# Performance work log

Hardware: AMD Instinct MI355X
Metric: run time of the kernel (lower is better)

Reference implementation:

```python
import jax, jax.numpy as jnp
import numpy as np
import math

N = 4096
E = 131072
IN_DIM, HID, OUT = 512, 256, 64
DEPTH = 3
RATIO = 0.5


def setup_inputs() -> dict:
    key = jax.random.key(0)
    ks = jax.random.split(key, 12)

    def w(k, fi, fo):
        return jax.random.normal(k, (fi, fo), jnp.float32) * (1.0 / np.sqrt(fi).astype(np.float32))

    return {
        "x": jax.random.normal(ks[0], (N, IN_DIM), jnp.float32),
        "edge_index": jax.random.randint(ks[1], (2, E), 0, N, jnp.int32),
        "dW0": w(ks[2], IN_DIM, HID), "dW1": w(ks[3], HID, HID),
        "dW2": w(ks[4], HID, HID), "dW3": w(ks[5], HID, HID),
        "db0": jnp.zeros((HID,), jnp.float32), "db1": jnp.zeros((HID,), jnp.float32),
        "db2": jnp.zeros((HID,), jnp.float32), "db3": jnp.zeros((HID,), jnp.float32),
        "pw0": jax.random.normal(ks[6], (HID,), jnp.float32),
        "pw1": jax.random.normal(ks[7], (HID,), jnp.float32),
        "pw2": jax.random.normal(ks[8], (HID,), jnp.float32),
        "uW0": w(ks[9], HID, HID), "uW1": w(ks[10], HID, HID), "uW2": w(ks[11], HID, OUT),
        "ub0": jnp.zeros((HID,), jnp.float32), "ub1": jnp.zeros((HID,), jnp.float32),
        "ub2": jnp.zeros((OUT,), jnp.float32),
    }


def gcn_conv(x, A, W, b):
    # GCNConv(improved=True): A_hat = A + 2I, sym-normalized.
    n = A.shape[0]
    eye = jnp.eye(n, dtype=A.dtype)
    Ah = A + 2.0 * eye
    d = Ah.sum(axis=1)
    dinv = jnp.where(d > 0, jax.lax.rsqrt(d), 0.0)
    An = dinv[:, None] * Ah * dinv[None, :]
    return An @ (x @ W) + b


def augment_adj(A):
    # add self loops, square the (weighted) adjacency, remove self loops
    n = A.shape[0]
    eye = jnp.eye(n, dtype=A.dtype)
    Al = A + eye
    A2 = Al @ Al
    return A2 * (1.0 - eye)


def topk_pool(x, A, w, k):
    # TopKPooling: score = tanh(x.w/||w||); keep top-k; gate kept features by score.
    score = jnp.tanh((x @ w) / jnp.linalg.norm(w))
    _, perm = jax.lax.top_k(score, k)
    xp = x[perm] * score[perm][:, None]
    return xp, A[perm][:, perm], perm


def _forward(x, edge_index, down_Ws, down_bs, pool_ws, up_Ws, up_bs):
    A = jnp.zeros((N, N), jnp.float32).at[edge_index[0], edge_index[1]].set(1.0)
    x = jax.nn.relu(gcn_conv(x, A, down_Ws[0], down_bs[0]))
    xs, As, perms = [x], [A], []
    n = N
    for i in range(1, DEPTH + 1):
        A = augment_adj(A)
        k = int(math.ceil(RATIO * n)); n = k
        x, A, perm = topk_pool(x, A, pool_ws[i - 1], k)
        x = jax.nn.relu(gcn_conv(x, A, down_Ws[i], down_bs[i]))
        if i < DEPTH:
            xs.append(x); As.append(A)
        perms.append(perm)
    for i in range(DEPTH):
        j = DEPTH - 1 - i
        res, A, perm = xs[j], As[j], perms[j]
        up = jnp.zeros_like(res).at[perm].set(x)   # unpool (sum_res=True)
        x = res + up
        x = gcn_conv(x, A, up_Ws[i], up_bs[i])
        if i < DEPTH - 1:
            x = jax.nn.relu(x)
    return x


def reference(x, edge_index, dW0, dW1, dW2, dW3, db0, db1, db2, db3,
              pw0, pw1, pw2, uW0, uW1, uW2, ub0, ub1, ub2):
    return _forward(x, edge_index,
                    [dW0, dW1, dW2, dW3], [db0, db1, db2, db3],
                    [pw0, pw1, pw2],
                    [uW0, uW1, uW2], [ub0, ub1, ub2])
```

## Files before the change

kernel.cpp:

```cpp
#include <hip/hip_runtime.h>
#include <math.h>

#define NN 4096
#define EE 131072
#define IN_DIM 512
#define HID 256
#define OUT_DIM 64
#define ECAP 128

typedef __attribute__((ext_vector_type(8))) short bf8_t;
typedef __attribute__((ext_vector_type(4))) float f4_t;
typedef __attribute__((ext_vector_type(8))) unsigned short us8_t;

#define GAS __attribute__((address_space(1)))
#define LAS __attribute__((address_space(3)))

__device__ __forceinline__ unsigned short f2bf(float v){
  union { float f; unsigned u; } x; x.f = v;
  unsigned r = x.u + 0x7fffu + ((x.u >> 16) & 1u);
  return (unsigned short)(r >> 16);
}
__device__ __forceinline__ float bf2f(unsigned short h){
  union { float f; unsigned u; } x; x.u = ((unsigned)h) << 16;
  return x.f;
}

__device__ __forceinline__ float waveReduceSum(float v){
#pragma unroll
  for (int off = 32; off > 0; off >>= 1) v += __shfl_down(v, off);
  return v;
}

__global__ __launch_bounds__(256) void k_prep(
    const float* __restrict__ x_in, const float* __restrict__ dW0,
    const float* __restrict__ dW1, const float* __restrict__ dW2,
    const float* __restrict__ dW3, const float* __restrict__ uW0,
    const float* __restrict__ uW1, const float* __restrict__ uW2,
    unsigned* __restrict__ bits,
    unsigned short* __restrict__ xinh, unsigned short* __restrict__ xinl,
    unsigned short* __restrict__ W0th, unsigned short* __restrict__ W0tl,
    unsigned short* __restrict__ W5th, unsigned short* __restrict__ W5tl,
    unsigned short* __restrict__ W2th, unsigned short* __restrict__ W2tl)
{
  int b = blockIdx.x;
  if (b < 128){
    int base = b * 4096 + threadIdx.x;
#pragma unroll
    for (int i = 0; i < 16; ++i) bits[base + i * 256] = 0;
    return;
  }
  b -= 128;
  if (b < 2048){
    int i0 = b * 1024 + threadIdx.x;
#pragma unroll
    for (int i = 0; i < 4; ++i){
      int idx = i0 + i * 256;
      float v = x_in[idx];
      unsigned short h = f2bf(v);
      xinh[idx] = h; xinl[idx] = f2bf(v - bf2f(h));
    }
    return;
  }
  b -= 2048;
  const float* X; unsigned short *Th, *Tl; int R, C, tile;
  if (b < 128){ X = dW0; Th = W0th; Tl = W0tl; R = 512; C = 256; tile = b; }
  else if (b < 448){
    int t2 = b - 128; int z = t2 >> 6; int rem = t2 & 63;
    const float* ws[5] = {dW1, dW2, dW3, uW0, uW1};
    X = ws[z]; Th = W5th + (size_t)z * 65536; Tl = W5tl + (size_t)z * 65536;
    R = 256; C = 256; tile = rem;
  } else { X = uW2; Th = W2th; Tl = W2tl; R = 256; C = 64; tile = b - 448; }
  int tpr = C >> 5;
  int bx = (tile % tpr) * 32, by = (tile / tpr) * 32;
  __shared__ float t[32][33];
  int tx = threadIdx.x & 31, ty = threadIdx.x >> 5;
#pragma unroll
  for (int i = 0; i < 4; ++i)
    t[ty + i * 8][tx] = X[(size_t)(by + ty + i * 8) * C + bx + tx];
  __syncthreads();
#pragma unroll
  for (int i = 0; i < 4; ++i){
    float v = t[tx][ty + i * 8];
    unsigned short h = f2bf(v);
    size_t o = (size_t)(bx + ty + i * 8) * R + by + tx;
    Th[o] = h; Tl[o] = f2bf(v - bf2f(h));
  }
}

__global__ void k_build_bits(const int* __restrict__ ei, unsigned* __restrict__ bits){
  int e = blockIdx.x * blockDim.x + threadIdx.x;
  if (e < EE){
    int r = ei[e], c = ei[EE + e];
    atomicOr(&bits[r * 128 + (c >> 5)], 1u << (c & 31));
  }
}

__global__ __launch_bounds__(128) void k_ell(const unsigned* __restrict__ bits,
                                             int* __restrict__ ell, int* __restrict__ cnt,
                                             float* __restrict__ dinv){
  int r = blockIdx.x, t = threadIdx.x;
  unsigned w = bits[r * 128 + t];
  int c = __popc(w);
  __shared__ int sc[128];
  sc[t] = c; __syncthreads();
  for (int off = 1; off < 128; off <<= 1){
    int a = sc[t], b = (t >= off) ? sc[t - off] : 0;
    __syncthreads(); sc[t] = a + b; __syncthreads();
  }
  int total = sc[127];
  int pos = sc[t] - c;
  int base = r * ECAP;
  while (w){
    int b = __ffs(w) - 1; w &= w - 1;
    if (pos < ECAP) ell[base + pos] = t * 32 + b;
    pos++;
  }
  if (t == 0){
    cnt[r] = (total < ECAP) ? total : ECAP;
    dinv[r] = 1.0f / sqrtf((float)total + 2.0f);
  }
}

template<int NCOLS, int RELU, int SC>
__global__ __launch_bounds__(256) void k_spmm_ell(
    const int* __restrict__ ell, const int* __restrict__ cnt,
    const float* __restrict__ Zs, const float* __restrict__ dinv,
    const float* __restrict__ bias, float* __restrict__ out,
    const float* __restrict__ scw, float* __restrict__ score)
{
  int r = blockIdx.x;
  __shared__ int s_idx[ECAP];
  __shared__ int s_n;
  __shared__ float sh[4 * NCOLS];
  __shared__ float sd[4], sq[4];
  if (threadIdx.x == 0) s_n = cnt[r];
  for (int i = threadIdx.x; i < ECAP; i += 256) s_idx[i] = ell[r * ECAP + i];
  __syncthreads();
  int n = s_n; if (n > ECAP) n = ECAP;
  int wv = threadIdx.x >> 6, lane = threadIdx.x & 63;
  if (NCOLS == 256){
    f4_t acc = (f4_t){0.f, 0.f, 0.f, 0.f};
    for (int e = wv; e < n; e += 4){
      const f4_t* row = (const f4_t*)(Zs + (size_t)s_idx[e] * 256);
      acc += row[lane];
    }
    ((f4_t*)(sh + wv * 256))[lane] = acc;
  } else {
    float acc = 0.f;
    for (int e = wv; e < n; e += 4)
      acc += Zs[(size_t)s_idx[e] * 64 + lane];
    sh[wv * 64 + lane] = acc;
  }
  __syncthreads();
  int t = threadIdx.x;
  float o = 0.f;
  if (t < NCOLS){
    float y = sh[t] + sh[NCOLS + t] + sh[2 * NCOLS + t] + sh[3 * NCOLS + t];
    float z = Zs[(size_t)r * NCOLS + t];
    o = dinv[r] * (y + 2.0f * z) + bias[t];
    if (RELU) o = fmaxf(o, 0.f);
    out[(size_t)r * NCOLS + t] = o;
  }
  if (SC){
    float w = scw[t];
    float d = waveReduceSum(o * w);
    float q = waveReduceSum(w * w);
    if (!lane){ sd[wv] = d; sq[wv] = q; }
    __syncthreads();
    if (!t) score[r] = tanhf((sd[0] + sd[1] + sd[2] + sd[3]) / sqrtf(sq[0] + sq[1] + sq[2] + sq[3]));
  }
}

__global__ __launch_bounds__(256) void k_pool_build(
    const float* __restrict__ x0, const float* __restrict__ score,
    const int* __restrict__ perm1, const int* __restrict__ inv1,
    const int* __restrict__ ell, const int* __restrict__ cnt,
    unsigned short* __restrict__ xph, unsigned short* __restrict__ xpl,
    unsigned char* __restrict__ Rb,
    unsigned short* __restrict__ xu1h, unsigned short* __restrict__ xu1l)
{
  int b = blockIdx.x;
  if (b < 2048){
    int pr = perm1[b]; float s = score[pr];
    int c = threadIdx.x;
    float v = x0[(size_t)pr * 256 + c] * s;
    unsigned short h = f2bf(v);
    xph[(size_t)b * 256 + c] = h;
    xpl[(size_t)b * 256 + c] = f2bf(v - bf2f(h));
    return;
  }
  if (b < 6144){
    int k = b - 2048;
    __shared__ unsigned char row[2048];
    for (int i = threadIdx.x; i < 512; i += 256) ((int*)row)[i] = 0;
    __syncthreads();
    int n = cnt[k];
    for (int e = threadIdx.x; e < n; e += 256){
      int s = inv1[ell[k * ECAP + e]];
      if (s >= 0) row[s] = 1;
    }
    __syncthreads();
    if (threadIdx.x == 0){
      int sk = inv1[k];
      if (sk >= 0) row[sk] += 1;
    }
    __syncthreads();
    *(uint2*)(Rb + (size_t)k * 2048 + threadIdx.x * 8) = *(uint2*)(row + threadIdx.x * 8);
    return;
  }
  int r = b - 6144;
  if (inv1[r] < 0){
    int c = threadIdx.x;
    float v = x0[(size_t)r * 256 + c];
    unsigned short h = f2bf(v);
    xu1h[(size_t)r * 256 + c] = h;
    xu1l[(size_t)r * 256 + c] = f2bf(v - bf2f(h));
  }
}

__global__ __launch_bounds__(256) void k_pool_fill(
    const float* __restrict__ x, const float* __restrict__ score,
    const int* __restrict__ perm, const int* __restrict__ inv, int k,
    unsigned short* __restrict__ xph, unsigned short* __restrict__ xpl,
    unsigned short* __restrict__ xuh, unsigned short* __restrict__ xul)
{
  int b = blockIdx.x, c = threadIdx.x;
  if (b < k){
    int pr = perm[b]; float s = score[pr];
    float v = x[(size_t)pr * 256 + c] * s;
    unsigned short h = f2bf(v);
    xph[(size_t)b * 256 + c] = h;
    xpl[(size_t)b * 256 + c] = f2bf(v - bf2f(h));
  } else {
    int r = b - k;
    if (inv[r] < 0){
      float v = x[(size_t)r * 256 + c];
      unsigned short h = f2bf(v);
      xuh[(size_t)r * 256 + c] = h;
      xul[(size_t)r * 256 + c] = f2bf(v - bf2f(h));
    }
  }
}

__global__ __launch_bounds__(256) void k_sq1(const int* __restrict__ ell, const int* __restrict__ cnt,
                                             const int* __restrict__ perm,
                                             const unsigned char* __restrict__ Rb,
                                             unsigned short* __restrict__ A1h,
                                             float* __restrict__ dinv1){
  int r = blockIdx.x;
  int pr = perm[r];
  __shared__ int s_idx[ECAP];
  __shared__ int s_n;
  __shared__ float sred[4];
  if (threadIdx.x == 0) s_n = cnt[pr];
  for (int i = threadIdx.x; i < ECAP; i += 256) s_idx[i] = ell[pr * ECAP + i];
  __syncthreads();
  int n = s_n; if (n > ECAP) n = ECAP;
  int colb = threadIdx.x * 8;
  uint2 acc = *(const uint2*)(Rb + (size_t)pr * 2048 + colb);
  for (int e = 0; e < n; ++e){
    uint2 v = *(const uint2*)(Rb + (size_t)s_idx[e] * 2048 + colb);
    acc.x += v.x; acc.y += v.y;
  }
  float fs = 0.f;
  us8_t o;
#pragma unroll
  for (int j = 0; j < 8; ++j){
    unsigned byte = ((j < 4 ? acc.x : acc.y) >> (8 * (j & 3))) & 0xFFu;
    if (colb + j == r) byte = 0;
    float f = (float)byte;
    fs += f;
    o[j] = f2bf(f);
  }
  *(us8_t*)(A1h + (size_t)r * 2048 + colb) = o;
  fs = waveReduceSum(fs);
  int lane = threadIdx.x & 63, wd = threadIdx.x >> 6;
  if (!lane) sred[wd] = fs;
  __syncthreads();
  if (!threadIdx.x)
    dinv1[r] = 1.0f / sqrtf(sred[0] + sred[1] + sred[2] + sred[3] + 2.0f);
}

template<int TWO>
__global__ __launch_bounds__(256) void k_tr_b(const unsigned short* __restrict__ Sh,
                                              const unsigned short* __restrict__ Sl,
                                              unsigned short* __restrict__ Dh,
                                              unsigned short* __restrict__ Dl, int R, int C){
  __shared__ unsigned short th[32][33];
  __shared__ unsigned short tl[TWO ? 32 : 1][TWO ? 33 : 1];
  int bx = blockIdx.x * 32, by = blockIdx.y * 32;
  int tx = threadIdx.x & 31, ty = threadIdx.x >> 5;
#pragma unroll
  for (int i = 0; i < 4; ++i){
    th[ty + i * 8][tx] = Sh[(size_t)(by + ty + i * 8) * C + bx + tx];
    if (TWO) tl[ty + i * 8][tx] = Sl[(size_t)(by + ty + i * 8) * C + bx + tx];
  }
  __syncthreads();
#pragma unroll
  for (int i = 0; i < 4; ++i){
    size_t o = (size_t)(bx + ty + i * 8) * R + by + tx;
    Dh[o] = th[tx][ty + i * 8];
    if (TWO) Dl[o] = tl[tx][ty + i * 8];
  }
}

template<int SRCL, int OUTL>
__global__ void k_grow2(const unsigned short* __restrict__ Sh, const unsigned short* __restrict__ Sl,
                        const unsigned short* __restrict__ Th, const unsigned short* __restrict__ Tl,
                        const int* __restrict__ perm,
                        unsigned short* __restrict__ Lh, unsigned short* __restrict__ Ll,
                        unsigned short* __restrict__ Rh, unsigned short* __restrict__ Rl,
                        int n, int half)
{
  int b = blockIdx.x;
  const unsigned short *sh, *sl; unsigned short *dh, *dl; int r;
  if (b < half){ r = b; sh = Sh; sl = Sl; dh = Lh; dl = Ll; }
  else { r = b - half; sh = Th; sl = Tl; dh = Rh; dl = Rl; }
  int pr = perm[r];
  for (int c = threadIdx.x; c < n; c += 256){
    float v = bf2f(sh[(size_t)pr * n + c]);
    if (SRCL) v += bf2f(sl[(size_t)pr * n + c]);
    if (pr == c) v += 1.f;
    unsigned short h = f2bf(v);
    dh[(size_t)r * n + c] = h;
    if (OUTL) dl[(size_t)r * n + c] = f2bf(v - bf2f(h));
  }
}

template<int HAS_AL, int HAS_BL, int HAS_LL, int EPI>
__global__ __launch_bounds__(256) void k_mm(
    const unsigned short* __restrict__ Ah, const unsigned short* __restrict__ Al,
    const unsigned short* __restrict__ Bh, const unsigned short* __restrict__ Bl,
    int M, int N, int K, int KS, float* __restrict__ P,
    float* __restrict__ Cf, unsigned short* __restrict__ Ch, unsigned short* __restrict__ Cl,
    const float* __restrict__ dinv)
{
  constexpr int NARR = 2 + HAS_AL + HAS_BL;
  constexpr int BUF = NARR * 8192;
  __shared__ int4 ldsq[NARR * 512 * 2];
  char* ldsc = (char*)ldsq;

  const int tid = threadIdx.x, lane = tid & 63, wid = tid >> 6;
  const int wm = wid >> 1, wn = wid & 1;
  const int bm = blockIdx.y << 6, bn = blockIdx.x << 6;
  const int z = blockIdx.z;
  const int l15 = lane & 15, l4 = lane >> 4;

  f4_t acc[2][2];
#pragma unroll
  for (int i = 0; i < 2; ++i)
#pragma unroll
    for (int j = 0; j < 2; ++j) acc[i][j] = (f4_t){0.f, 0.f, 0.f, 0.f};

  const size_t rb = (size_t)K * 2;
  const size_t kz = (size_t)z * KS * 2;
  const char* pAh = (const char*)Ah + (size_t)bm * rb;
  const char* pAl = HAS_AL ? (const char*)Al + (size_t)bm * rb : nullptr;
  const char* pBh = (const char*)Bh + (size_t)bn * rb;
  const char* pBl = HAS_BL ? (const char*)Bl + (size_t)bn * rb : nullptr;

  auto stage = [&](int t, int b2){
    char* ldsb = ldsc + b2 * BUF;
    const size_t kb = kz + (size_t)t * 128;
#pragma unroll
    for (int it = 0; it < 2; ++it){
      const int idx = tid + (it << 8);
      const int row = idx >> 3;
      const int kc = ((idx & 7) << 4) ^ ((row & 7) << 4);
      const size_t go = (size_t)row * rb + kb + kc;
      const int lo = idx * 16;
      __builtin_amdgcn_global_load_lds((const GAS void*)(pAh + go), (LAS void*)(ldsb + lo), 16, 0, 0);
      __builtin_amdgcn_global_load_lds((const GAS void*)(pBh + go), (LAS void*)(ldsb + 8192 + lo), 16, 0, 0);
      if (HAS_AL)
        __builtin_amdgcn_global_load_lds((const GAS void*)(pAl + go), (LAS void*)(ldsb + 16384 + lo), 16, 0, 0);
      if (HAS_BL)
        __builtin_amdgcn_global_load_lds((const GAS void*)(pBl + go), (LAS void*)(ldsb + (2 + HAS_AL) * 8192 + lo), 16, 0, 0);
    }
  };

  const int T = KS >> 6;
  stage(0, 0);
  int b = 0;
  for (int t = 0; t < T; ++t){
    if (t + 1 < T){
      stage(t + 1, b ^ 1);
      if constexpr (NARR == 2) asm volatile("s_waitcnt vmcnt(4)" ::: "memory");
      else if constexpr (NARR == 3) asm volatile("s_waitcnt vmcnt(6)" ::: "memory");
      else asm volatile("s_waitcnt vmcnt(8)" ::: "memory");
    } else {
      asm volatile("s_waitcnt vmcnt(0)" ::: "memory");
    }
    __syncthreads();
    const char* ldsb = ldsc + b * BUF;
#pragma unroll
    for (int ks = 0; ks < 2; ++ks){
      bf8_t aH[2], aL[2], bH[2], bL[2];
#pragma unroll
      for (int f = 0; f < 2; ++f){
        int ar = wm * 32 + f * 16 + l15;
        int aoff = ar * 128 + (((ks * 64) + (l4 << 4)) ^ ((ar & 7) << 4));
        aH[f] = *(const bf8_t*)(ldsb + aoff);
        if (HAS_AL) aL[f] = *(const bf8_t*)(ldsb + 16384 + aoff);
        int br = wn * 32 + f * 16 + l15;
        int boff = br * 128 + (((ks * 64) + (l4 << 4)) ^ ((br & 7) << 4));
        bH[f] = *(const bf8_t*)(ldsb + 8192 + boff);
        if (HAS_BL) bL[f] = *(const bf8_t*)(ldsb + (2 + HAS_AL) * 8192 + boff);
      }
#pragma unroll
      for (int i = 0; i < 2; ++i)
#pragma unroll
        for (int j = 0; j < 2; ++j){
          acc[i][j] = __builtin_amdgcn_mfma_f32_16x16x32_bf16(aH[i], bH[j], acc[i][j], 0, 0, 0);
          if (HAS_BL) acc[i][j] = __builtin_amdgcn_mfma_f32_16x16x32_bf16(aH[i], bL[j], acc[i][j], 0, 0, 0);
          if (HAS_AL) acc[i][j] = __builtin_amdgcn_mfma_f32_16x16x32_bf16(aL[i], bH[j], acc[i][j], 0, 0, 0);
          if (HAS_LL) acc[i][j] = __builtin_amdgcn_mfma_f32_16x16x32_bf16(aL[i], bL[j], acc[i][j], 0, 0, 0);
        }
    }
    __syncthreads();
    b ^= 1;
  }

  float* Pz = (EPI == 0) ? P + (size_t)z * M * N : nullptr;
#pragma unroll
  for (int i = 0; i < 2; ++i)
#pragma unroll
    for (int j = 0; j < 2; ++j)
#pragma unroll
      for (int r = 0; r < 4; ++r){
        int grow = bm + wm * 32 + i * 16 + l4 * 4 + r;
        int gcol = bn + wn * 32 + j * 16 + l15;
        float v = acc[i][j][r];
        size_t o = (size_t)grow * N + gcol;
        if (EPI == 0){
          Pz[o] = v;
        } else if (EPI == 2){
          Cf[o] = dinv[grow] * v;
        } else {
          float sv = dinv[grow] * v;
          Cf[o] = sv;
          unsigned short h = f2bf(sv);
          size_t ot = (size_t)gcol * M + grow;
          Ch[ot] = h; Cl[ot] = f2bf(sv - bf2f(h));
        }
      }
}

template<int EPI, int SC>
__global__ __launch_bounds__(256) void k_red(
    const float* __restrict__ P, int Z, int M, int NC,
    const float* __restrict__ dinv, const float* __restrict__ Zs,
    const float* __restrict__ bias,
    float* __restrict__ Of, unsigned short* __restrict__ Oh, unsigned short* __restrict__ Ol,
    float* __restrict__ dout, int relu,
    const float* __restrict__ scw, float* __restrict__ score,
    const float* __restrict__ res, const int* __restrict__ permsel)
{
  int row = blockIdx.x;
  int prow = (EPI == 4) ? permsel[row] : 0;
  float rsum = 0.f;
  float o_sc = 0.f;
  for (int c = threadIdx.x; c < NC; c += 256){
    size_t o = (size_t)row * NC + c;
    float s = P[o];
    for (int zz = 1; zz < Z; ++zz) s += P[(size_t)zz * M * NC + o];
    if (EPI == 2){
      float out = dinv[row] * (s + 2.0f * Zs[o]) + bias[c];
      if (relu) out = fmaxf(out, 0.f);
      Of[o] = out;
      o_sc = out;
    } else if (EPI == 3){
      float v = (c == row) ? 0.f : s;
      unsigned short h = f2bf(v);
      Oh[o] = h; Ol[o] = f2bf(v - bf2f(h));
      rsum += v;
    } else {
      float out = dinv[row] * (s + 2.0f * Zs[o]) + bias[c];
      if (relu) out = fmaxf(out, 0.f);
      float comb = res[(size_t)prow * NC + c] + out;
      unsigned short h = f2bf(comb);
      size_t od = (size_t)prow * NC + c;
      Oh[od] = h; Ol[od] = f2bf(comb - bf2f(h));
    }
  }
  int lane = threadIdx.x & 63, wd = threadIdx.x >> 6;
  if (EPI == 3){
    rsum = waveReduceSum(rsum);
    __shared__ float sr[4];
    if (!lane) sr[wd] = rsum;
    __syncthreads();
    if (!threadIdx.x) dout[row] = 1.0f / sqrtf(sr[0] + sr[1] + sr[2] + sr[3] + 2.0f);
  }
  if (SC){
    float w = scw[threadIdx.x];
    float d = waveReduceSum(o_sc * w);
    float q = waveReduceSum(w * w);
    __shared__ float sd[4], sq[4];
    if (!lane){ sd[wd] = d; sq[wd] = q; }
    __syncthreads();
    if (!threadIdx.x)
      score[row] = tanhf((sd[0] + sd[1] + sd[2] + sd[3]) / sqrtf(sq[0] + sq[1] + sq[2] + sq[3]));
  }
}

__global__ void k_topk(const float* __restrict__ score, int n, int k,
                       int* __restrict__ perm, int* __restrict__ inv){
  int i = blockIdx.x; float si = score[i];
  int cnt = 0;
  for (int j = threadIdx.x; j < n; j += 256){
    float sj = score[j];
    if (sj > si || (sj == si && j < i)) cnt++;
  }
#pragma unroll
  for (int off = 32; off > 0; off >>= 1) cnt += __shfl_down(cnt, off);
  __shared__ int sh[4];
  int lane = threadIdx.x & 63, wid = threadIdx.x >> 6;
  if (lane == 0) sh[wid] = cnt;
  __syncthreads();
  if (threadIdx.x == 0){
    int rank = sh[0] + sh[1] + sh[2] + sh[3];
    if (rank < k){ perm[rank] = i; inv[i] = rank; }
    else inv[i] = -1;
  }
}

extern "C" void kernel_launch(void* const* d_in, const int* in_sizes, int n_in,
                              void* d_out, int out_size, void* d_ws, size_t ws_size,
                              hipStream_t stream){
  (void)in_sizes; (void)n_in; (void)out_size;
  const float* x_in = (const float*)d_in[0];
  const int*   ei   = (const int*)d_in[1];
  const float* dW0 = (const float*)d_in[2];
  const float* dW1 = (const float*)d_in[3];
  const float* dW2 = (const float*)d_in[4];
  const float* dW3 = (const float*)d_in[5];
  const float* db0 = (const float*)d_in[6];
  const float* db1 = (const float*)d_in[7];
  const float* db2 = (const float*)d_in[8];
  const float* db3 = (const float*)d_in[9];
  const float* pw0 = (const float*)d_in[10];
  const float* pw1 = (const float*)d_in[11];
  const float* pw2 = (const float*)d_in[12];
  const float* uW0 = (const float*)d_in[13];
  const float* uW1 = (const float*)d_in[14];
  const float* uW2 = (const float*)d_in[15];
  const float* ub0 = (const float*)d_in[16];
  const float* ub1 = (const float*)d_in[17];
  const float* ub2 = (const float*)d_in[18];

  char* p = (char*)d_ws;
  auto alloc = [&](size_t nbytes) -> void* {
    void* q = (void*)p; p += (nbytes + 255) & ~(size_t)255; return q;
  };
  unsigned* bits = (unsigned*)alloc((size_t)4096 * 128 * 4);
  int* ell = (int*)alloc((size_t)4096 * ECAP * 4);
  int* cnt = (int*)alloc(4096 * 4);
  int* inv1 = (int*)alloc(4096 * 4);
  int* inv2 = (int*)alloc(2048 * 4);
  int* inv3 = (int*)alloc(1024 * 4);
  unsigned char* Rb = (unsigned char*)alloc((size_t)4096 * 2048);
  float* Pp = (float*)alloc((size_t)8 * 1024 * 1024);
  unsigned short* A1h = (unsigned short*)alloc((size_t)2048 * 2048 * 2);
  unsigned short* A1T = (unsigned short*)alloc((size_t)2048 * 2048 * 2);
  unsigned short* A2h = (unsigned short*)alloc((size_t)1024 * 1024 * 2);
  unsigned short* A2l = (unsigned short*)alloc((size_t)1024 * 1024 * 2);
  unsigned short* A2Th = (unsigned short*)alloc((size_t)1024 * 1024 * 2);
  unsigned short* A2Tl = (unsigned short*)alloc((size_t)1024 * 1024 * 2);
  unsigned short* A3h = (unsigned short*)alloc((size_t)512 * 512 * 2);
  unsigned short* A3l = (unsigned short*)alloc((size_t)512 * 512 * 2);
  unsigned short* Lb2h = (unsigned short*)alloc((size_t)1024 * 2048 * 2);
  unsigned short* Rt2h = (unsigned short*)alloc((size_t)1024 * 2048 * 2);
  unsigned short* Lb3h = (unsigned short*)alloc((size_t)512 * 1024 * 2);
  unsigned short* Lb3l = (unsigned short*)alloc((size_t)512 * 1024 * 2);
  unsigned short* Rt3h = (unsigned short*)alloc((size_t)512 * 1024 * 2);
  unsigned short* Rt3l = (unsigned short*)alloc((size_t)512 * 1024 * 2);
  unsigned short* xinh = (unsigned short*)alloc((size_t)4096 * 512 * 2);
  unsigned short* xinl = (unsigned short*)alloc((size_t)4096 * 512 * 2);
  float* x0 = (float*)alloc((size_t)4096 * HID * 4);
  float* x1 = (float*)alloc((size_t)2048 * HID * 4);
  float* x2 = (float*)alloc((size_t)1024 * HID * 4);
  unsigned short* xu1h = (unsigned short*)alloc((size_t)4096 * HID * 2);
  unsigned short* xu1l = (unsigned short*)alloc((size_t)4096 * HID * 2);
  unsigned short* xu2h = (unsigned short*)alloc((size_t)2048 * HID * 2);
  unsigned short* xu2l = (unsigned short*)alloc((size_t)2048 * HID * 2);
  unsigned short* xu3h = (unsigned short*)alloc((size_t)1024 * HID * 2);
  unsigned short* xu3l = (unsigned short*)alloc((size_t)1024 * HID * 2);
  unsigned short* xph = (unsigned short*)alloc((size_t)2048 * HID * 2);
  unsigned short* xpl = (unsigned short*)alloc((size_t)2048 * HID * 2);
  unsigned short* W0th = (unsigned short*)alloc((size_t)256 * 512 * 2);
  unsigned short* W0tl = (unsigned short*)alloc((size_t)256 * 512 * 2);
  unsigned short* W5th = (unsigned short*)alloc((size_t)5 * 256 * 256 * 2);
  unsigned short* W5tl = (unsigned short*)alloc((size_t)5 * 256 * 256 * 2);
  unsigned short* W2th = (unsigned short*)alloc((size_t)64 * 256 * 2);
  unsigned short* W2tl = (unsigned short*)alloc((size_t)64 * 256 * 2);
  float* Zs  = (float*)alloc((size_t)4096 * HID * 4);
  unsigned short* ZsTh = (unsigned short*)alloc((size_t)256 * 2048 * 2);
  unsigned short* ZsTl = (unsigned short*)alloc((size_t)256 * 2048 * 2);
  float* dinv0 = (float*)alloc(4096 * 4);
  float* dinv1 = (float*)alloc(2048 * 4);
  float* dinv2 = (float*)alloc(1024 * 4);
  float* dinv3 = (float*)alloc(512 * 4);
  float* score = (float*)alloc(4096 * 4);
  int* perm1 = (int*)alloc(2048 * 4);
  int* perm2 = (int*)alloc(1024 * 4);
  int* perm3 = (int*)alloc(512 * 4);
  if ((size_t)(p - (char*)d_ws) > ws_size) return;

  k_prep<<<2640, 256, 0, stream>>>(x_in, dW0, dW1, dW2, dW3, uW0, uW1, uW2, bits,
                                   xinh, xinl, W0th, W0tl, W5th, W5tl, W2th, W2tl);
  k_build_bits<<<EE / 256, 256, 0, stream>>>(ei, bits);
  k_ell<<<4096, 128, 0, stream>>>(bits, ell, cnt, dinv0);

  { dim3 g(4, 64);
    k_mm<1,1,0,2><<<g, 256, 0, stream>>>(xinh, xinl, W0th, W0tl, 4096, HID, IN_DIM, IN_DIM,
                                         nullptr, Zs, nullptr, nullptr, dinv0); }
  k_spmm_ell<256,1,1><<<4096, 256, 0, stream>>>(ell, cnt, Zs, dinv0, db0, x0, pw0, score);

  k_topk<<<4096, 256, 0, stream>>>(score, 4096, 2048, perm1, inv1);
  k_pool_build<<<10240, 256, 0, stream>>>(x0, score, perm1, inv1, ell, cnt,
                                          xph, xpl, Rb, xu1h, xu1l);
  k_sq1<<<2048, 256, 0, stream>>>(ell, cnt, perm1, Rb, A1h, dinv1);
  { dim3 g(4, 32);
    k_mm<1,1,0,4><<<g, 256, 0, stream>>>(xph, xpl, W5th, W5tl, 2048, HID, HID, HID,
                                         nullptr, Zs, ZsTh, ZsTl, dinv1); }
  { dim3 g(4, 32, 4);
    k_mm<0,1,0,0><<<g, 256, 0, stream>>>(A1h, nullptr, ZsTh, ZsTl, 2048, HID, 2048, 512,
                                         Pp, nullptr, nullptr, nullptr, nullptr); }
  k_red<2,1><<<2048, 256, 0, stream>>>(Pp, 4, 2048, 256, dinv1, Zs, db1,
                                       x1, nullptr, nullptr, nullptr, 1, pw1, score, nullptr, nullptr);

  k_topk<<<2048, 256, 0, stream>>>(score, 2048, 1024, perm2, inv2);
  { dim3 g(64, 64); k_tr_b<0><<<g, 256, 0, stream>>>(A1h, nullptr, A1T, nullptr, 2048, 2048); }
  k_grow2<0,0><<<2048, 256, 0, stream>>>(A1h, nullptr, A1T, nullptr, perm2,
                                         Lb2h, nullptr, Rt2h, nullptr, 2048, 1024);
  { dim3 g(16, 16, 2);
    k_mm<0,0,0,0><<<g, 256, 0, stream>>>(Lb2h, nullptr, Rt2h, nullptr, 1024, 1024, 2048, 1024,
                                         Pp, nullptr, nullptr, nullptr, nullptr); }
  k_red<3,0><<<1024, 256, 0, stream>>>(Pp, 2, 1024, 1024, nullptr, nullptr, nullptr,
                                       nullptr, A2h, A2l, dinv2, 0, nullptr, nullptr, nullptr, nullptr);
  k_pool_fill<<<3072, 256, 0, stream>>>(x1, score, perm2, inv2, 1024, xph, xpl, xu2h, xu2l);
  { dim3 g(4, 16);
    k_mm<1,1,0,4><<<g, 256, 0, stream>>>(xph, xpl, W5th + 65536, W5tl + 65536, 1024, HID, HID, HID,
                                         nullptr, Zs, ZsTh, ZsTl, dinv2); }
  { dim3 g(4, 16, 4);
    k_mm<1,1,0,0><<<g, 256, 0, stream>>>(A2h, A2l, ZsTh, ZsTl, 1024, HID, 1024, 256,
                                         Pp, nullptr, nullptr, nullptr, nullptr); }
  k_red<2,1><<<1024, 256, 0, stream>>>(Pp, 4, 1024, 256, dinv2, Zs, db2,
                                       x2, nullptr, nullptr, nullptr, 1, pw2, score, nullptr, nullptr);

  k_topk<<<1024, 256, 0, stream>>>(score, 1024, 512, perm3, inv3);
  { dim3 g(32, 32); k_tr_b<1><<<g, 256, 0, stream>>>(A2h, A2l, A2Th, A2Tl, 1024, 1024); }
  k_grow2<1,1><<<1024, 256, 0, stream>>>(A2h, A2l, A2Th, A2Tl, perm3,
                                         Lb3h, Lb3l, Rt3h, Rt3l, 1024, 512);
  { dim3 g(8, 8, 4);
    k_mm<1,1,1,0><<<g, 256, 0, stream>>>(Lb3h, Lb3l, Rt3h, Rt3l, 512, 512, 1024, 256,
                                         Pp, nullptr, nullptr, nullptr, nullptr); }
  k_red<3,0><<<512, 256, 0, stream>>>(Pp, 4, 512, 512, nullptr, nullptr, nullptr,
                                      nullptr, A3h, A3l, dinv3, 0, nullptr, nullptr, nullptr, nullptr);
  k_pool_fill<<<1536, 256, 0, stream>>>(x2, score, perm3, inv3, 512, xph, xpl, xu3h, xu3l);
  { dim3 g(4, 8);
    k_mm<1,1,0,4><<<g, 256, 0, stream>>>(xph, xpl, W5th + 2 * 65536, W5tl + 2 * 65536, 512, HID, HID, HID,
                                         nullptr, Zs, ZsTh, ZsTl, dinv3); }
  { dim3 g(4, 8, 4);
    k_mm<1,1,0,0><<<g, 256, 0, stream>>>(A3h, A3l, ZsTh, ZsTl, 512, HID, 512, 128,
                                         Pp, nullptr, nullptr, nullptr, nullptr); }
  k_red<4,0><<<512, 256, 0, stream>>>(Pp, 4, 512, 256, dinv3, Zs, db3,
                                      nullptr, xu3h, xu3l, nullptr, 1, nullptr, nullptr, x2, perm3);

  { dim3 g(4, 16);
    k_mm<1,1,0,4><<<g, 256, 0, stream>>>(xu3h, xu3l, W5th + 3 * 65536, W5tl + 3 * 65536, 1024, HID, HID, HID,
                                         nullptr, Zs, ZsTh, ZsTl, dinv2); }
  { dim3 g(4, 16, 4);
    k_mm<1,1,0,0><<<g, 256, 0, stream>>>(A2h, A2l, ZsTh, ZsTl, 1024, HID, 1024, 256,
                                         Pp, nullptr, nullptr, nullptr, nullptr); }
  k_red<4,0><<<1024, 256, 0, stream>>>(Pp, 4, 1024, 256, dinv2, Zs, ub0,
                                       nullptr, xu2h, xu2l, nullptr, 1, nullptr, nullptr, x1, perm2);

  { dim3 g(4, 32);
    k_mm<1,1,0,4><<<g, 256, 0, stream>>>(xu2h, xu2l, W5th + 4 * 65536, W5tl + 4 * 65536, 2048, HID, HID, HID,
                                         nullptr, Zs, ZsTh, ZsTl, dinv1); }
  { dim3 g(4, 32, 4);
    k_mm<0,1,0,0><<<g, 256, 0, stream>>>(A1h, nullptr, ZsTh, ZsTl, 2048, HID, 2048, 512,
                                         Pp, nullptr, nullptr, nullptr, nullptr); }
  k_red<4,0><<<2048, 256, 0, stream>>>(Pp, 4, 2048, 256, dinv1, Zs, ub1,
                                       nullptr, xu1h, xu1l, nullptr, 1, nullptr, nullptr, x0, perm1);

  { dim3 g(1, 64);
    k_mm<1,1,0,2><<<g, 256, 0, stream>>>(xu1h, xu1l, W2th, W2tl, 4096, OUT_DIM, HID, HID,
                                         nullptr, Zs, nullptr, nullptr, dinv0); }
  k_spmm_ell<64,0,0><<<4096, 256, 0, stream>>>(ell, cnt, Zs, dinv0, ub2, (float*)d_out, nullptr, nullptr);
}
```

Before: 243.8 us.

## Fuse pool fill, transpose and row/col gather into one kernel; vectorize reductions

Replaces the separate full-matrix transpose, the row/column gather kernel and the pool-fill kernel with a single k_pp kernel. It gathers rows directly and writes the permuted transposed columns from tiled reads, so the full transposed adjacency copy is never materialized. It also rewrites k_red to handle one row per wavefront with float4 loads, removing shared-memory block reductions and cutting the grid size by four. The fused kernel has heterogeneous block roles and scattered column writes, and it moves the pool fill earlier, before the squaring matmul.

```diff
diff --git a/kernel.cpp b/kernel.cpp
--- a/kernel.cpp
+++ b/kernel.cpp
@@ -11,6 +11,7 @@
 typedef __attribute__((ext_vector_type(8))) short bf8_t;
 typedef __attribute__((ext_vector_type(4))) float f4_t;
 typedef __attribute__((ext_vector_type(8))) unsigned short us8_t;
+typedef __attribute__((ext_vector_type(4))) unsigned short us4_t;
 
 #define GAS __attribute__((address_space(1)))
 #define LAS __attribute__((address_space(3)))
@@ -218,12 +219,18 @@
   }
 }
 
-__global__ __launch_bounds__(256) void k_pool_fill(
+template<int SRCL, int OUTL>
+__global__ __launch_bounds__(256) void k_pp(
     const float* __restrict__ x, const float* __restrict__ score,
-    const int* __restrict__ perm, const int* __restrict__ inv, int k,
+    const int* __restrict__ perm, const int* __restrict__ inv, int n, int k,
     unsigned short* __restrict__ xph, unsigned short* __restrict__ xpl,
-    unsigned short* __restrict__ xuh, unsigned short* __restrict__ xul)
+    unsigned short* __restrict__ xuh, unsigned short* __restrict__ xul,
+    const unsigned short* __restrict__ Ah, const unsigned short* __restrict__ Al,
+    unsigned short* __restrict__ Lh, unsigned short* __restrict__ Ll,
+    unsigned short* __restrict__ Rh, unsigned short* __restrict__ Rl)
 {
+  __shared__ float t[32][33];
+  __shared__ int sinv[32];
   int b = blockIdx.x, c = threadIdx.x;
   if (b < k){
     int pr = perm[b]; float s = score[pr];
@@ -231,13 +238,56 @@
     unsigned short h = f2bf(v);
     xph[(size_t)b * 256 + c] = h;
     xpl[(size_t)b * 256 + c] = f2bf(v - bf2f(h));
-  } else {
-    int r = b - k;
-    if (inv[r] < 0){
-      float v = x[(size_t)r * 256 + c];
+    return;
+  }
+  b -= k;
+  if (b < n){
+    if (inv[b] < 0){
+      float v = x[(size_t)b * 256 + c];
       unsigned short h = f2bf(v);
-      xuh[(size_t)r * 256 + c] = h;
-      xul[(size_t)r * 256 + c] = f2bf(v - bf2f(h));
+      xuh[(size_t)b * 256 + c] = h;
+      xul[(size_t)b * 256 + c] = f2bf(v - bf2f(h));
+    }
+    return;
+  }
+  b -= n;
+  if (b < k){
+    int r = b, pr = perm[r];
+    for (int cc = threadIdx.x; cc < n; cc += 256){
+      float v = bf2f(Ah[(size_t)pr * n + cc]);
+      if (SRCL) v += bf2f(Al[(size_t)pr * n + cc]);
+      if (pr == cc) v += 1.f;
+      unsigned short h = f2bf(v);
+      Lh[(size_t)r * n + cc] = h;
+      if (OUTL) Ll[(size_t)r * n + cc] = f2bf(v - bf2f(h));
+    }
+    return;
+  }
+  b -= k;
+  int tpr = n >> 5;
+  int kt = b / tpr, ct = b - kt * tpr;
+  int tx = threadIdx.x & 31, ty = threadIdx.x >> 5;
+  if (threadIdx.x < 32) sinv[threadIdx.x] = inv[ct * 32 + threadIdx.x];
+#pragma unroll
+  for (int i = 0; i < 4; ++i){
+    int kl = ty + i * 8;
+    size_t src = (size_t)(kt * 32 + kl) * n + ct * 32 + tx;
+    float v = bf2f(Ah[src]);
+    if (SRCL) v += bf2f(Al[src]);
+    t[kl][tx] = v;
+  }
+  __syncthreads();
+#pragma unroll
+  for (int i = 0; i < 4; ++i){
+    int cl = ty + i * 8;
+    int s = sinv[cl];
+    if (s >= 0){
+      float v = t[tx][cl];
+      if (kt * 32 + tx == ct * 32 + cl) v += 1.f;
+      unsigned short h = f2bf(v);
+      size_t o = (size_t)s * n + kt * 32 + tx;
+      Rh[o] = h;
+      if (OUTL) Rl[o] = f2bf(v - bf2f(h));
     }
   }
 }
@@ -281,52 +331,6 @@
     dinv1[r] = 1.0f / sqrtf(sred[0] + sred[1] + sred[2] + sred[3] + 2.0f);
 }
 
-template<int TWO>
-__global__ __launch_bounds__(256) void k_tr_b(const unsigned short* __restrict__ Sh,
-                                              const unsigned short* __restrict__ Sl,
-                                              unsigned short* __restrict__ Dh,
-                                              unsigned short* __restrict__ Dl, int R, int C){
-  __shared__ unsigned short th[32][33];
-  __shared__ unsigned short tl[TWO ? 32 : 1][TWO ? 33 : 1];
-  int bx = blockIdx.x * 32, by = blockIdx.y * 32;
-  int tx = threadIdx.x & 31, ty = threadIdx.x >> 5;
-#pragma unroll
-  for (int i = 0; i < 4; ++i){
-    th[ty + i * 8][tx] = Sh[(size_t)(by + ty + i * 8) * C + bx + tx];
-    if (TWO) tl[ty + i * 8][tx] = Sl[(size_t)(by + ty + i * 8) * C + bx + tx];
-  }
-  __syncthreads();
-#pragma unroll
-  for (int i = 0; i < 4; ++i){
-    size_t o = (size_t)(bx + ty + i * 8) * R + by + tx;
-    Dh[o] = th[tx][ty + i * 8];
-    if (TWO) Dl[o] = tl[tx][ty + i * 8];
-  }
-}
-
-template<int SRCL, int OUTL>
-__global__ void k_grow2(const unsigned short* __restrict__ Sh, const unsigned short* __restrict__ Sl,
-                        const unsigned short* __restrict__ Th, const unsigned short* __restrict__ Tl,
-                        const int* __restrict__ perm,
-                        unsigned short* __restrict__ Lh, unsigned short* __restrict__ Ll,
-                        unsigned short* __restrict__ Rh, unsigned short* __restrict__ Rl,
-                        int n, int half)
-{
-  int b = blockIdx.x;
-  const unsigned short *sh, *sl; unsigned short *dh, *dl; int r;
-  if (b < half){ r = b; sh = Sh; sl = Sl; dh = Lh; dl = Ll; }
-  else { r = b - half; sh = Th; sl = Tl; dh = Rh; dl = Rl; }
-  int pr = perm[r];
-  for (int c = threadIdx.x; c < n; c += 256){
-    float v = bf2f(sh[(size_t)pr * n + c]);
-    if (SRCL) v += bf2f(sl[(size_t)pr * n + c]);
-    if (pr == c) v += 1.f;
-    unsigned short h = f2bf(v);
-    dh[(size_t)r * n + c] = h;
-    if (OUTL) dl[(size_t)r * n + c] = f2bf(v - bf2f(h));
-  }
-}
-
 template<int HAS_AL, int HAS_BL, int HAS_LL, int EPI>
 __global__ __launch_bounds__(256) void k_mm(
     const unsigned short* __restrict__ Ah, const unsigned short* __restrict__ Al,
@@ -455,50 +459,68 @@
     const float* __restrict__ scw, float* __restrict__ score,
     const float* __restrict__ res, const int* __restrict__ permsel)
 {
-  int row = blockIdx.x;
+  int w = threadIdx.x >> 6, lane = threadIdx.x & 63;
+  int row = blockIdx.x * 4 + w;
   int prow = (EPI == 4) ? permsel[row] : 0;
-  float rsum = 0.f;
-  float o_sc = 0.f;
-  for (int c = threadIdx.x; c < NC; c += 256){
-    size_t o = (size_t)row * NC + c;
-    float s = P[o];
-    for (int zz = 1; zz < Z; ++zz) s += P[(size_t)zz * M * NC + o];
+  float di = (EPI != 3) ? dinv[row] : 0.f;
+  float rsum = 0.f, o_d = 0.f, o_q = 0.f;
+  for (int c0 = lane * 4; c0 < NC; c0 += 256){
+    size_t o = (size_t)row * NC + c0;
+    f4_t s = *(const f4_t*)(P + o);
+    for (int zz = 1; zz < Z; ++zz) s += *(const f4_t*)(P + (size_t)zz * M * NC + o);
     if (EPI == 2){
-      float out = dinv[row] * (s + 2.0f * Zs[o]) + bias[c];
-      if (relu) out = fmaxf(out, 0.f);
-      Of[o] = out;
-      o_sc = out;
+      f4_t z4 = *(const f4_t*)(Zs + o);
+      f4_t b4 = *(const f4_t*)(bias + c0);
+      f4_t out;
+#pragma unroll
+      for (int j = 0; j < 4; ++j){
+        float v = di * (s[j] + 2.0f * z4[j]) + b4[j];
+        if (relu) v = fmaxf(v, 0.f);
+        out[j] = v;
+      }
+      *(f4_t*)(Of + o) = out;
+      if (SC){
+        f4_t w4 = *(const f4_t*)(scw + c0);
+#pragma unroll
+        for (int j = 0; j < 4; ++j){ o_d += out[j] * w4[j]; o_q += w4[j] * w4[j]; }
+      }
     } else if (EPI == 3){
-      float v = (c == row) ? 0.f : s;
-      unsigned short h = f2bf(v);
-      Oh[o] = h; Ol[o] = f2bf(v - bf2f(h));
-      rsum += v;
+      us4_t h4, l4v;
+#pragma unroll
+      for (int j = 0; j < 4; ++j){
+        float v = (c0 + j == row) ? 0.f : s[j];
+        unsigned short h = f2bf(v);
+        h4[j] = h; l4v[j] = f2bf(v - bf2f(h));
+        rsum += v;
+      }
+      *(us4_t*)(Oh + o) = h4;
+      *(us4_t*)(Ol + o) = l4v;
     } else {
-      float out = dinv[row] * (s + 2.0f * Zs[o]) + bias[c];
-      if (relu) out = fmaxf(out, 0.f);
-      float comb = res[(size_t)prow * NC + c] + out;
-      unsigned short h = f2bf(comb);
-      size_t od = (size_t)prow * NC + c;
-      Oh[od] = h; Ol[od] = f2bf(comb - bf2f(h));
-    }
-  }
-  int lane = threadIdx.x & 63, wd = threadIdx.x >> 6;
+      f4_t z4 = *(const f4_t*)(Zs + o);
+      f4_t b4 = *(const f4_t*)(bias + c0);
+      f4_t r4 = *(const f4_t*)(res + (size_t)prow * NC + c0);
+      us4_t h4, l4v;
+#pragma unroll
+      for (int j = 0; j < 4; ++j){
+        float v = di * (s[j] + 2.0f * z4[j]) + b4[j];
+        if (relu) v = fmaxf(v, 0.f);
+        float comb = r4[j] + v;
+        unsigned short h = f2bf(comb);
+        h4[j] = h; l4v[j] = f2bf(comb - bf2f(h));
+      }
+      size_t od = (size_t)prow * NC + c0;
+      *(us4_t*)(Oh + od) = h4;
+      *(us4_t*)(Ol + od) = l4v;
+    }
+  }
   if (EPI == 3){
     rsum = waveReduceSum(rsum);
-    __shared__ float sr[4];
-    if (!lane) sr[wd] = rsum;
-    __syncthreads();
-    if (!threadIdx.x) dout[row] = 1.0f / sqrtf(sr[0] + sr[1] + sr[2] + sr[3] + 2.0f);
+    if (!lane) dout[row] = 1.0f / sqrtf(rsum + 2.0f);
   }
   if (SC){
-    float w = scw[threadIdx.x];
-    float d = waveReduceSum(o_sc * w);
-    float q = waveReduceSum(w * w);
-    __shared__ float sd[4], sq[4];
-    if (!lane){ sd[wd] = d; sq[wd] = q; }
-    __syncthreads();
-    if (!threadIdx.x)
-      score[row] = tanhf((sd[0] + sd[1] + sd[2] + sd[3]) / sqrtf(sq[0] + sq[1] + sq[2] + sq[3]));
+    o_d = waveReduceSum(o_d);
+    o_q = waveReduceSum(o_q);
+    if (!lane) score[row] = tanhf(o_d / sqrtf(o_q));
   }
 }
 
@@ -560,11 +582,8 @@
   unsigned char* Rb = (unsigned char*)alloc((size_t)4096 * 2048);
   float* Pp = (float*)alloc((size_t)8 * 1024 * 1024);
   unsigned short* A1h = (unsigned short*)alloc((size_t)2048 * 2048 * 2);
-  unsigned short* A1T = (unsigned short*)alloc((size_t)2048 * 2048 * 2);
   unsigned short* A2h = (unsigned short*)alloc((size_t)1024 * 1024 * 2);
   unsigned short* A2l = (unsigned short*)alloc((size_t)1024 * 1024 * 2);
-  unsigned short* A2Th = (unsigned short*)alloc((size_t)1024 * 1024 * 2);
-  unsigned short* A2Tl = (unsigned short*)alloc((size_t)1024 * 1024 * 2);
   unsigned short* A3h = (unsigned short*)alloc((size_t)512 * 512 * 2);
   unsigned short* A3l = (unsigned short*)alloc((size_t)512 * 512 * 2);
   unsigned short* Lb2h = (unsigned short*)alloc((size_t)1024 * 2048 * 2);
@@ -625,45 +644,43 @@
   { dim3 g(4, 32, 4);
     k_mm<0,1,0,0><<<g, 256, 0, stream>>>(A1h, nullptr, ZsTh, ZsTl, 2048, HID, 2048, 512,
                                          Pp, nullptr, nullptr, nullptr, nullptr); }
-  k_red<2,1><<<2048, 256, 0, stream>>>(Pp, 4, 2048, 256, dinv1, Zs, db1,
-                                       x1, nullptr, nullptr, nullptr, 1, pw1, score, nullptr, nullptr);
+  k_red<2,1><<<512, 256, 0, stream>>>(Pp, 4, 2048, 256, dinv1, Zs, db1,
+                                      x1, nullptr, nullptr, nullptr, 1, pw1, score, nullptr, nullptr);
 
   k_topk<<<2048, 256, 0, stream>>>(score, 2048, 1024, perm2, inv2);
-  { dim3 g(64, 64); k_tr_b<0><<<g, 256, 0, stream>>>(A1h, nullptr, A1T, nullptr, 2048, 2048); }
-  k_grow2<0,0><<<2048, 256, 0, stream>>>(A1h, nullptr, A1T, nullptr, perm2,
-                                         Lb2h, nullptr, Rt2h, nullptr, 2048, 1024);
+  k_pp<0,0><<<8192, 256, 0, stream>>>(x1, score, perm2, inv2, 2048, 1024,
+                                      xph, xpl, xu2h, xu2l, A1h, nullptr,
+                                      Lb2h, nullptr, Rt2h, nullptr);
   { dim3 g(16, 16, 2);
     k_mm<0,0,0,0><<<g, 256, 0, stream>>>(Lb2h, nullptr, Rt2h, nullptr, 1024, 1024, 2048, 1024,
                                          Pp, nullptr, nullptr, nullptr, nullptr); }
-  k_red<3,0><<<1024, 256, 0, stream>>>(Pp, 2, 1024, 1024, nullptr, nullptr, nullptr,
-                                       nullptr, A2h, A2l, dinv2, 0, nullptr, nullptr, nullptr, nullptr);
-  k_pool_fill<<<3072, 256, 0, stream>>>(x1, score, perm2, inv2, 1024, xph, xpl, xu2h, xu2l);
+  k_red<3,0><<<256, 256, 0, stream>>>(Pp, 2, 1024, 1024, nullptr, nullptr, nullptr,
+                                      nullptr, A2h, A2l, dinv2, 0, nullptr, nullptr, nullptr, nullptr);
   { dim3 g(4, 16);
     k_mm<1,1,0,4><<<g, 256, 0, stream>>>(xph, xpl, W5th + 65536, W5tl + 65536, 1024, HID, HID, HID,
                                          nullptr, Zs, ZsTh, ZsTl, dinv2); }
   { dim3 g(4, 16, 4);
     k_mm<1,1,0,0><<<g, 256, 0, stream>>>(A2h, A2l, ZsTh, ZsTl, 1024, HID, 1024, 256,
                                          Pp, nullptr, nullptr, nullptr, nullptr); }
-  k_red<2,1><<<1024, 256, 0, stream>>>(Pp, 4, 1024, 256, dinv2, Zs, db2,
-                                       x2, nullptr, nullptr, nullptr, 1, pw2, score, nullptr, nullptr);
+  k_red<2,1><<<256, 256, 0, stream>>>(Pp, 4, 1024, 256, dinv2, Zs, db2,
+                                      x2, nullptr, nullptr, nullptr, 1, pw2, score, nullptr, nullptr);
 
   k_topk<<<1024, 256, 0, stream>>>(score, 1024, 512, perm3, inv3);
-  { dim3 g(32, 32); k_tr_b<1><<<g, 256, 0, stream>>>(A2h, A2l, A2Th, A2Tl, 1024, 1024); }
-  k_grow2<1,1><<<1024, 256, 0, stream>>>(A2h, A2l, A2Th, A2Tl, perm3,
-                                         Lb3h, Lb3l, Rt3h, Rt3l, 1024, 512);
+  k_pp<1,1><<<3072, 256, 0, stream>>>(x2, score, perm3, inv3, 1024, 512,
+                                      xph, xpl, xu3h, xu3l, A2h, A2l,
+                                      Lb3h, Lb3l, Rt3h, Rt3l);
   { dim3 g(8, 8, 4);
     k_mm<1,1,1,0><<<g, 256, 0, stream>>>(Lb3h, Lb3l, Rt3h, Rt3l, 512, 512, 1024, 256,
                                          Pp, nullptr, nullptr, nullptr, nullptr); }
-  k_red<3,0><<<512, 256, 0, stream>>>(Pp, 4, 512, 512, nullptr, nullptr, nullptr,
+  k_red<3,0><<<128, 256, 0, stream>>>(Pp, 4, 512, 512, nullptr, nullptr, nullptr,
                                       nullptr, A3h, A3l, dinv3, 0, nullptr, nullptr, nullptr, nullptr);
-  k_pool_fill<<<1536, 256, 0, stream>>>(x2, score, perm3, inv3, 512, xph, xpl, xu3h, xu3l);
   { dim3 g(4, 8);
     k_mm<1,1,0,4><<<g, 256, 0, stream>>>(xph, xpl, W5th + 2 * 65536, W5tl + 2 * 65536, 512, HID, HID, HID,
                                          nullptr, Zs, ZsTh, ZsTl, dinv3); }
   { dim3 g(4, 8, 4);
     k_mm<1,1,0,0><<<g, 256, 0, stream>>>(A3h, A3l, ZsTh, ZsTl, 512, HID, 512, 128,
                                          Pp, nullptr, nullptr, nullptr, nullptr); }
-  k_red<4,0><<<512, 256, 0, stream>>>(Pp, 4, 512, 256, dinv3, Zs, db3,
+  k_red<4,0><<<128, 256, 0, stream>>>(Pp, 4, 512, 256, dinv3, Zs, db3,
                                       nullptr, xu3h, xu3l, nullptr, 1, nullptr, nullptr, x2, perm3);
 
   { dim3 g(4, 16);
@@ -672,8 +689,8 @@
   { dim3 g(4, 16, 4);
     k_mm<1,1,0,0><<<g, 256, 0, stream>>>(A2h, A2l, ZsTh, ZsTl, 1024, HID, 1024, 256,
                                          Pp, nullptr, nullptr, nullptr, nullptr); }
-  k_red<4,0><<<1024, 256, 0, stream>>>(Pp, 4, 1024, 256, dinv2, Zs, ub0,
-                                       nullptr, xu2h, xu2l, nullptr, 1, nullptr, nullptr, x1, perm2);
+  k_red<4,0><<<256, 256, 0, stream>>>(Pp, 4, 1024, 256, dinv2, Zs, ub0,
+                                      nullptr, xu2h, xu2l, nullptr, 1, nullptr, nullptr, x1, perm2);
 
   { dim3 g(4, 32);
     k_mm<1,1,0,4><<<g, 256, 0, stream>>>(xu2h, xu2l, W5th + 4 * 65536, W5tl + 4 * 65536, 2048, HID, HID, HID,
@@ -681,8 +698,8 @@
   { dim3 g(4, 32, 4);
     k_mm<0,1,0,0><<<g, 256, 0, stream>>>(A1h, nullptr, ZsTh, ZsTl, 2048, HID, 2048, 512,
                                          Pp, nullptr, nullptr, nullptr, nullptr); }
-  k_red<4,0><<<2048, 256, 0, stream>>>(Pp, 4, 2048, 256, dinv1, Zs, ub1,
-                                       nullptr, xu1h, xu1l, nullptr, 1, nullptr, nullptr, x0, perm1);
+  k_red<4,0><<<512, 256, 0, stream>>>(Pp, 4, 2048, 256, dinv1, Zs, ub1,
+                                      nullptr, xu1h, xu1l, nullptr, 1, nullptr, nullptr, x0, perm1);
 
   { dim3 g(1, 64);
     k_mm<1,1,0,2><<<g, 256, 0, stream>>>(xu1h, xu1l, W2th, W2tl, 4096, OUT_DIM, HID, HID,
```

Result: faster. 232.5 us (-4.6%).
